# Kernel optimization log

Measured on AMD Instinct MI355X. Metric: run time of the kernel, lower is better.

## Reference

```python
import jax, jax.numpy as jnp
import numpy as np

INPUT_DIM = 64
OUTPUT_DIM = 128
KNN = 10          # hardcoded min(10, N) in source
RADIUS = 0.02     # density radius in source


def setup_inputs() -> dict:
    key = jax.random.key(0)
    k1, k2, k3, k4, k5, k6, k7 = jax.random.split(key, 7)
    B, N = 2, 8192
    points = jax.random.uniform(k1, (B, N, 3), dtype=jnp.float32)
    features = jax.random.normal(k2, (B, N, INPUT_DIM), dtype=jnp.float32)
    leaf_mask = jax.random.randint(k3, (B, N), 0, 2) > 0
    d_in = INPUT_DIM + 6
    s1 = 1.0 / np.sqrt(d_in)
    s2 = 1.0 / np.sqrt(OUTPUT_DIM)
    W1 = jax.random.uniform(k4, (d_in, OUTPUT_DIM), jnp.float32, -s1, s1)
    b1 = jax.random.uniform(k5, (OUTPUT_DIM,), jnp.float32, -s1, s1)
    W2 = jax.random.uniform(k6, (OUTPUT_DIM, OUTPUT_DIM), jnp.float32, -s2, s2)
    b2 = jax.random.uniform(k7, (OUTPUT_DIM,), jnp.float32, -s2, s2)
    return {"points": points, "features": features, "leaf_mask": leaf_mask,
            "W1": W1, "b1": b1, "W2": W2, "b2": b2}


def _leaf_geometry(points, mask):
    # points: [N,3], mask: [N] bool -> [N,6]
    mask_f = mask.astype(points.dtype)
    cnt = jnp.maximum(mask_f.sum(), 1.0)
    center = (points * mask_f[:, None]).sum(0) / cnt      # mean of masked points
    rel = points - center                                  # [N,3]
    dist_c = jnp.linalg.norm(rel, axis=1)                  # dist to leaf center
    rel_h = rel[:, 2]                                      # relative height
    horiz = jnp.linalg.norm(rel[:, :2], axis=1)            # horizontal distance
    # pairwise euclidean distances [N,N]; used only for thresholding and knn
    sq = jnp.sum(points * points, axis=1)
    d2 = sq[:, None] + sq[None, :] - 2.0 * (points @ points.T)
    dist = jax.lax.stop_gradient(jnp.sqrt(jnp.maximum(d2, 0.0)))
    density = jnp.sum((dist < RADIUS) & mask[None, :], axis=1).astype(points.dtype)
    # KNN (smallest distances, includes self) -> local PCA curvature
    _, idx = jax.lax.top_k(-dist, KNN)                     # [N,KNN]
    neighbors = points[idx]                                # [N,KNN,3]
    centered = neighbors - points[:, None, :]
    cov = jnp.einsum('nki,nkj->nij', centered, centered) / float(KNN)  # [N,3,3]
    ev = jnp.linalg.eigh(cov)[0]                           # ascending eigenvalues
    curv = ev[:, 0] / (ev[:, 2] + 1e-8)
    rad = jnp.arctan2(rel[:, 1], rel[:, 0])
    geom = jnp.stack([dist_c, rel_h, horiz, density, curv, rad], axis=1)
    # source returns zeros when mask is empty
    return jnp.where(mask_f.sum() > 0, geom, jnp.zeros_like(geom))


def reference(points, features, leaf_mask, W1, b1, W2, b2):
    geom = jax.vmap(_leaf_geometry)(points, leaf_mask)     # [B,N,6]
    combined = jnp.concatenate([features, geom], axis=-1)  # [B,N,input_dim+6]
    h = jax.nn.relu(combined @ W1 + b1)
    return jax.nn.relu(h @ W2 + b2)                        # [B,N,output_dim]
```

## Files before the change

kernel.cpp:

```cpp
#include <hip/hip_runtime.h>
#include <math.h>
#include <stdint.h>

#define B_SZ   2
#define N_PTS  8192
#define IN_DIM 64
#define D_IN   70
#define ODIM   128
#define NQ_ALL (B_SZ * N_PTS)
#define RADIUS_F 0.02f

#define GDIM  32
#define NCELL (GDIM * GDIM * GDIM)
#define HCELL 0.03125f

#define SUP     4
#define NSUP_AX 8
#define NSUPER  (NSUP_AX * NSUP_AX * NSUP_AX)
#define SCAP    352
#define LCAP    24
#define MAXROWS 100

#define MROWS   16

typedef unsigned long long u64;

__device__ __forceinline__ void insert11(u64 (&best)[11], u64 key) {
#pragma unroll
  for (int j = 10; j >= 1; --j) {
    u64 hi = (best[j - 1] > key) ? best[j - 1] : key;
    best[j] = (best[j] < hi) ? best[j] : hi;
  }
  best[0] = (best[0] < key) ? best[0] : key;
}
__device__ __forceinline__ void insert10(u64 (&best)[10], u64 key) {
#pragma unroll
  for (int j = 9; j >= 1; --j) {
    u64 hi = (best[j - 1] > key) ? best[j - 1] : key;
    best[j] = (best[j] < hi) ? best[j] : hi;
  }
  best[0] = (best[0] < key) ? best[0] : key;
}

__device__ __forceinline__ float sq3(float x, float y, float z) {
  return __fadd_rn(__fadd_rn(__fmul_rn(x, x), __fmul_rn(y, y)), __fmul_rn(z, z));
}

__device__ __forceinline__ int cellOf(float v) {
  int c = (int)(v * 32.0f);
  return min(max(c, 0), GDIM - 1);
}

__device__ __forceinline__ void geom_epilogue(const float* __restrict__ P,
                                              const int (&idxs)[10], float dens,
                                              float px, float py, float pz,
                                              float4 ctr, float* __restrict__ g) {
  double c00 = 0, c01 = 0, c02 = 0, c11 = 0, c12 = 0, c22 = 0;
#pragma unroll
  for (int j = 0; j < 10; ++j) {
    const int idx = idxs[j];
    const float nx = P[3 * idx + 0], ny = P[3 * idx + 1], nz = P[3 * idx + 2];
    const float ex = __fsub_rn(nx, px);
    const float ey = __fsub_rn(ny, py);
    const float ez = __fsub_rn(nz, pz);
    c00 += (double)ex * ex; c01 += (double)ex * ey; c02 += (double)ex * ez;
    c11 += (double)ey * ey; c12 += (double)ey * ez; c22 += (double)ez * ez;
  }
  const double a00 = c00 / 10.0, a01 = c01 / 10.0, a02 = c02 / 10.0;
  const double a11 = c11 / 10.0, a12 = c12 / 10.0, a22 = c22 / 10.0;

  double p1 = a01 * a01 + a02 * a02 + a12 * a12;
  double qq = (a00 + a11 + a22) / 3.0;
  double p2 = (a00 - qq) * (a00 - qq) + (a11 - qq) * (a11 - qq) +
              (a22 - qq) * (a22 - qq) + 2.0 * p1;
  double ev0, ev2;
  if (p2 <= 1e-60) {
    ev0 = ev2 = qq;
  } else {
    double p = sqrt(p2 / 6.0);
    double invp = 1.0 / p;
    double b00 = (a00 - qq) * invp, b11 = (a11 - qq) * invp, b22 = (a22 - qq) * invp;
    double b01 = a01 * invp, b02 = a02 * invp, b12 = a12 * invp;
    double detB = b00 * (b11 * b22 - b12 * b12) - b01 * (b01 * b22 - b12 * b02) +
                  b02 * (b01 * b12 - b11 * b02);
    double r = 0.5 * detB;
    r = fmin(1.0, fmax(-1.0, r));
    double phi = acos(r) / 3.0;
    ev2 = qq + 2.0 * p * cos(phi);
    ev0 = qq + 2.0 * p * cos(phi + 2.0943951023931953);
  }
  const float curv = (float)(ev0 / (ev2 + 1e-08));

  const bool on = ctr.w > 0.0f;
  const float rx = __fsub_rn(px, ctr.x);
  const float ry = __fsub_rn(py, ctr.y);
  const float rz = __fsub_rn(pz, ctr.z);
  const float dist_c = sqrtf(sq3(rx, ry, rz));
  const float horiz  = sqrtf(__fadd_rn(__fmul_rn(rx, rx), __fmul_rn(ry, ry)));
  const float rad    = atan2f(ry, rx);

  g[0] = on ? dist_c : 0.0f;
  g[1] = on ? rz : 0.0f;
  g[2] = on ? horiz : 0.0f;
  g[3] = on ? dens : 0.0f;
  g[4] = on ? curv : 0.0f;
  g[5] = on ? rad : 0.0f;
}

__global__ __launch_bounds__(256) void k_build(const float* __restrict__ points,
                                               const int* __restrict__ mask,
                                               int* __restrict__ count,
                                               double* __restrict__ ctrAcc) {
  const int t = blockIdx.x * 256 + threadIdx.x;
  const int b = t >> 13;
  const int i = t & (N_PTS - 1);
  const float* P = points + (size_t)b * N_PTS * 3;
  const float x = P[3 * i + 0], y = P[3 * i + 1], z = P[3 * i + 2];
  atomicAdd(&count[b * NCELL + (cellOf(z) * GDIM + cellOf(y)) * GDIM + cellOf(x)], 1);

  const bool m = mask[b * N_PTS + i] != 0;
  double vx = m ? (double)x : 0.0, vy = m ? (double)y : 0.0;
  double vz = m ? (double)z : 0.0, vc = m ? 1.0 : 0.0;
#pragma unroll
  for (int s = 1; s < 64; s <<= 1) {
    vx += __shfl_xor(vx, s); vy += __shfl_xor(vy, s);
    vz += __shfl_xor(vz, s); vc += __shfl_xor(vc, s);
  }
  __shared__ double sh[4][4];
  const int w = threadIdx.x >> 6;
  if ((threadIdx.x & 63) == 0) { sh[0][w] = vx; sh[1][w] = vy; sh[2][w] = vz; sh[3][w] = vc; }
  __syncthreads();
  if (threadIdx.x == 0) {
    atomicAdd(&ctrAcc[b * 4 + 0], sh[0][0] + sh[0][1] + sh[0][2] + sh[0][3]);
    atomicAdd(&ctrAcc[b * 4 + 1], sh[1][0] + sh[1][1] + sh[1][2] + sh[1][3]);
    atomicAdd(&ctrAcc[b * 4 + 2], sh[2][0] + sh[2][1] + sh[2][2] + sh[2][3]);
    atomicAdd(&ctrAcc[b * 4 + 3], sh[3][0] + sh[3][1] + sh[3][2] + sh[3][3]);
  }
}

__global__ __launch_bounds__(1024) void k_scan(const int* __restrict__ count,
                                               int* __restrict__ start,
                                               int* __restrict__ cur,
                                               const double* __restrict__ ctrAcc,
                                               float* __restrict__ centerOut) {
  const int b = blockIdx.x;
  const int t = threadIdx.x;
  if (t == 0) {
    const float cf = (float)ctrAcc[b * 4 + 3];
    const float div = fmaxf(cf, 1.0f);
    centerOut[b * 4 + 0] = (float)ctrAcc[b * 4 + 0] / div;
    centerOut[b * 4 + 1] = (float)ctrAcc[b * 4 + 1] / div;
    centerOut[b * 4 + 2] = (float)ctrAcc[b * 4 + 2] / div;
    centerOut[b * 4 + 3] = (cf > 0.0f) ? 1.0f : 0.0f;
  }
  int c[32]; int sum = 0;
#pragma unroll
  for (int j = 0; j < 32; ++j) { c[j] = count[b * NCELL + t * 32 + j]; sum += c[j]; }
  __shared__ int s[1024];
  s[t] = sum;
  __syncthreads();
  for (int off = 1; off < 1024; off <<= 1) {
    int v = (t >= off) ? s[t - off] : 0;
    __syncthreads();
    if (t >= off) s[t] += v;
    __syncthreads();
  }
  int excl = (t > 0) ? s[t - 1] : 0;
#pragma unroll
  for (int j = 0; j < 32; ++j) {
    start[b * (NCELL + 1) + t * 32 + j] = excl;
    cur[b * NCELL + t * 32 + j] = excl;
    excl += c[j];
  }
  if (t == 1023) start[b * (NCELL + 1) + NCELL] = excl;
}

__global__ __launch_bounds__(256) void k_scatter(const float* __restrict__ points,
                                                 const int* __restrict__ mask,
                                                 int* __restrict__ cur,
                                                 float4* __restrict__ sorted) {
  const int t = blockIdx.x * 256 + threadIdx.x;
  const int b = t >> 13;
  const int i = t & (N_PTS - 1);
  const float* P = points + (size_t)b * N_PTS * 3;
  const float x = P[3 * i + 0], y = P[3 * i + 1], z = P[3 * i + 2];
  const int cell = (cellOf(z) * GDIM + cellOf(y)) * GDIM + cellOf(x);
  const int pos = atomicAdd(&cur[b * NCELL + cell], 1);
  const unsigned wb = (unsigned)i | ((mask[b * N_PTS + i] != 0) ? 0x80000000u : 0u);
  sorted[(size_t)b * N_PTS + pos] = make_float4(x, y, z, __uint_as_float(wb));
}

__global__ __launch_bounds__(128) void k_collect(const float* __restrict__ points,
                                                 const float4* __restrict__ sorted,
                                                 const int* __restrict__ start,
                                                 const float* __restrict__ center,
                                                 float* __restrict__ geom,
                                                 int* __restrict__ list,
                                                 int* __restrict__ listCnt,
                                                 float DENS_T) {
  const int b  = blockIdx.y;
  const int sc = blockIdx.x;
  const int sx = sc & 7, sy = (sc >> 3) & 7, sz = sc >> 6;
  const int tid = threadIdx.x;

  const int* ST = start + b * (NCELL + 1);
  const float4* SP = sorted + (size_t)b * N_PTS;

  const int x0 = SUP * sx, x1 = SUP * sx + SUP - 1;
  const int y0 = SUP * sy, y1 = SUP * sy + SUP - 1;
  const int z0 = SUP * sz, z1 = SUP * sz + SUP - 1;
  const int hx0 = max(x0 - 3, 0), hx1 = min(x1 + 3, GDIM - 1);
  const int hy0 = max(y0 - 3, 0), hy1 = min(y1 + 3, GDIM - 1);
  const int hz0 = max(z0 - 3, 0), hz1 = min(z1 + 3, GDIM - 1);
  const int yc = hy1 - hy0 + 1;
  const int R  = (hz1 - hz0 + 1) * yc;

  __shared__ int    rs[MAXROWS], rp[MAXROWS + 1];
  __shared__ int    qs_[16], qp_[17];
  __shared__ float4 pts4[SCAP];
  __shared__ u64    lbuf[128 * LCAP];

  if (tid < 64) {
    {
      int qlen = 0, qst = 0;
      if (tid < 16) {
        const int z = z0 + (tid >> 2), y = y0 + (tid & 3);
        const int base = (z * GDIM + y) * GDIM;
        qst  = ST[base + x0];
        qlen = ST[base + x1 + 1] - qst;
      }
      int inc = qlen;
      for (int off = 1; off < 64; off <<= 1) { int v = __shfl_up(inc, off); if (tid >= off) inc += v; }
      if (tid < 16) { qs_[tid] = qst; qp_[tid] = inc - qlen; }
      if (tid == 63) qp_[16] = inc;
    }
    {
      int len[2] = {0, 0}, st2[2] = {0, 0};
#pragma unroll
      for (int k = 0; k < 2; ++k) {
        const int r = tid * 2 + k;
        if (r < R) {
          const int z = hz0 + r / yc, y = hy0 + r % yc;
          const int base = (z * GDIM + y) * GDIM;
          st2[k] = ST[base + hx0];
          len[k] = ST[base + hx1 + 1] - st2[k];
        }
      }
      int sum = len[0] + len[1];
      int inc = sum;
      for (int off = 1; off < 64; off <<= 1) { int v = __shfl_up(inc, off); if (tid >= off) inc += v; }
      int exc = inc - sum;
#pragma unroll
      for (int k = 0; k < 2; ++k) {
        const int r = tid * 2 + k;
        if (r < R) { rs[r] = st2[k]; rp[r] = exc; }
        exc += len[k];
      }
      if (tid == 63) rp[R] = inc;
    }
  }
  __syncthreads();

  const int C    = rp[R];
  const int qtot = qp_[16];
  if (qtot == 0) return;

  if (C > SCAP) {
    for (int t = tid; t < qtot; t += 128) {
      int lo = 0, hi = 15;
      while (lo < hi) { const int mid = (lo + hi + 1) >> 1; if (qp_[mid] <= t) lo = mid; else hi = mid - 1; }
      const int qglob = qs_[lo] + (t - qp_[lo]);
      const int pos = atomicAdd(listCnt, 1);
      list[pos] = (b << 13) | qglob;
    }
    return;
  }

  for (int i = tid; i < C; i += 128) {
    int lo = 0, hi = R - 1;
    while (lo < hi) { const int mid = (lo + hi + 1) >> 1; if (rp[mid] <= i) lo = mid; else hi = mid - 1; }
    pts4[i] = SP[rs[lo] + (i - rp[lo])];
  }
  __syncthreads();

  const bool cxl = (x0 - 3 < 0), cxh = (x1 + 3 > GDIM - 1);
  const bool cyl = (y0 - 3 < 0), cyh = (y1 + 3 > GDIM - 1);
  const bool czl = (z0 - 3 < 0), czh = (z1 + 3 > GDIM - 1);

  const float4 ctr = reinterpret_cast<const float4*>(center)[b];
  const float* P = points + (size_t)b * N_PTS * 3;
  const int sub = tid & 3;
  const int gq  = tid >> 2;

  for (int q0 = 0; q0 < qtot; q0 += 32) {
    const int myq = q0 + gq;
    const bool act = (myq < qtot);
    const int mq = act ? myq : 0;
    int lo = 0, hi = 15;
    while (lo < hi) { const int mid = (lo + hi + 1) >> 1; if (qp_[mid] <= mq) lo = mid; else hi = mid - 1; }
    const int qglob = qs_[lo] + (mq - qp_[lo]);
    const float4 qp4 = SP[qglob];
    const int qidx = (int)(__float_as_uint(qp4.w) & 0x7FFFFFFFu);
    const float px = qp4.x, py = qp4.y, pz = qp4.z;
    const float sqq = sq3(px, py, pz);

    const float mxl = cxl ? 1e9f : __fsub_rn(px, (float)hx0 * HCELL);
    const float mxh = cxh ? 1e9f : __fsub_rn((float)(hx1 + 1) * HCELL, px);
    const float myl = cyl ? 1e9f : __fsub_rn(py, (float)hy0 * HCELL);
    const float myh = cyh ? 1e9f : __fsub_rn((float)(hy1 + 1) * HCELL, py);
    const float mzl = czl ? 1e9f : __fsub_rn(pz, (float)hz0 * HCELL);
    const float mzh = czh ? 1e9f : __fsub_rn((float)(hz1 + 1) * HCELL, pz);
    const float gr = fminf(fminf(fminf(mxl, mxh), fminf(myl, myh)), fminf(mzl, mzh));
    const float fx = 0.5f * (1.0f + fminf(fminf(px, 1.0f - px) * (1.0f / 0.0935f), 1.0f));
    const float fy = 0.5f * (1.0f + fminf(fminf(py, 1.0f - py) * (1.0f / 0.0935f), 1.0f));
    const float fz = 0.5f * (1.0f + fminf(fminf(pz, 1.0f - pz) * (1.0f / 0.0935f), 1.0f));
    const float rT = 0.0935f * cbrtf(1.0f / (fx * fy * fz));
    const float cR = fminf(gr, rT);
    const float cT2 = cR * cR;
    const float certR = cR * 0.999f;

    int cnt = 0;
    u64* myb = &lbuf[tid * LCAP];
#pragma unroll 2
    for (int j = sub; j < C; j += 4) {
      const float4 tp = pts4[j];
      const float sqc = sq3(tp.x, tp.y, tp.z);
      const float dot = __fmaf_rn(pz, tp.z, __fmaf_rn(py, tp.y, __fmul_rn(px, tp.x)));
      const float d2  = __fsub_rn(__fadd_rn(sqq, sqc), __fmul_rn(2.0f, dot));
      const float d2c = fmaxf(d2, 0.0f);
      if (d2c < cT2) {
        if (cnt < LCAP) {
          const unsigned wb = __float_as_uint(tp.w);
          myb[cnt] = ((u64)__float_as_uint(d2c) << 32)
                   | (u64)(((wb & 0x7FFFFFFFu) << 1) | (wb >> 31));
        }
        ++cnt;
      }
    }

    u64 best[11];
#pragma unroll
    for (int j = 0; j < 11; ++j) best[j] = ~0ull;
    float dens = 0.0f;
    const int m = min(cnt, LCAP);
    for (int i = 0; i < m; ++i) {
      const u64 e = myb[i];
      if ((e & 1ull) && __uint_as_float((unsigned)(e >> 32)) < DENS_T) dens += 1.0f;
      if (e < best[10]) insert11(best, e);
    }
    int cntg = cnt;
    int over = (cnt > LCAP) ? 1 : 0;
#pragma unroll
    for (int s = 1; s < 4; s <<= 1) {
      dens += __shfl_xor(dens, s);
      cntg += __shfl_xor(cntg, s);
      over |= __shfl_xor(over, s);
      u64 ok[11];
#pragma unroll
      for (int j = 0; j < 11; ++j) ok[j] = __shfl_xor(best[j], s);
#pragma unroll
      for (int j = 0; j < 11; ++j) {
        if (ok[j] < best[10]) insert11(best, ok[j]); else break;
      }
    }

    if (act && sub == 0) {
      const float dist9 = sqrtf(__uint_as_float((unsigned)(best[9] >> 32)));
      bool bad = (over != 0) || (cntg < 10) || !(dist9 < certR);
      if (cntg >= 11) {
        const float dist10 = sqrtf(__uint_as_float((unsigned)(best[10] >> 32)));
        bad = bad || (dist10 == dist9);
      }
      if (bad) {
        const int pos = atomicAdd(listCnt, 1);
        list[pos] = (b << 13) | qglob;
      } else {
        int idxs[10];
#pragma unroll
        for (int j = 0; j < 10; ++j) idxs[j] = (int)(((unsigned)best[j]) >> 1);
        geom_epilogue(P, idxs, dens, px, py, pz, ctr,
                      geom + ((size_t)b * N_PTS + qidx) * 6);
      }
    }
  }
}

__global__ __launch_bounds__(256) void k_wavefb(const float* __restrict__ points,
                                                const float4* __restrict__ sorted,
                                                const int* __restrict__ start,
                                                const float* __restrict__ center,
                                                float* __restrict__ geom,
                                                int* __restrict__ flags2,
                                                const int* __restrict__ list,
                                                const int* __restrict__ listCnt) {
  const int lane = threadIdx.x & 63;
  const int wid  = threadIdx.x >> 6;
  const int n = *listCnt;
  for (int it = blockIdx.x * 4 + wid; it < n; it += gridDim.x * 4) {
    const int e = list[it];
    const int b = e >> 13, qs = e & (N_PTS - 1);
    const float4* SP = sorted + (size_t)b * N_PTS;
    const int* ST = start + b * (NCELL + 1);
    const float4 qp = SP[qs];
    const int qidx = (int)(__float_as_uint(qp.w) & 0x7FFFFFFFu);
    const float px = qp.x, py = qp.y, pz = qp.z;
    const float sqq = sq3(px, py, pz);
    const int cx = cellOf(px), cy = cellOf(py), cz = cellOf(pz);
    const int xlo = max(cx - 8, 0), xhi = min(cx + 8, GDIM - 1);
    const int ylo = max(cy - 8, 0), yhi = min(cy + 8, GDIM - 1);
    const int zlo = max(cz - 8, 0), zhi = min(cz + 8, GDIM - 1);
    const int ycw = yhi - ylo + 1;
    const int Rw = (zhi - zlo + 1) * ycw;

    u64 best[10];
#pragma unroll
    for (int j = 0; j < 10; ++j) best[j] = ((u64)0x7F800000u << 32) | 0xFFFFFFFFu;
    float dens = 0.0f;

    for (int r = lane; r < Rw; r += 64) {
      const int z = zlo + r / ycw, y = ylo + r % ycw;
      const int base = (z * GDIM + y) * GDIM;
      const int j0 = ST[base + xlo], j1 = ST[base + xhi + 1];
      for (int j = j0; j < j1; ++j) {
        const float4 tp = SP[j];
        const unsigned wb = __float_as_uint(tp.w);
        const float sqc = sq3(tp.x, tp.y, tp.z);
        const float dot = __fmaf_rn(pz, tp.z, __fmaf_rn(py, tp.y, __fmul_rn(px, tp.x)));
        const float d2  = __fsub_rn(__fadd_rn(sqq, sqc), __fmul_rn(2.0f, dot));
        const float dist = sqrtf(fmaxf(d2, 0.0f));
        if ((dist < RADIUS_F) && (wb & 0x80000000u)) dens += 1.0f;
        const u64 key = ((u64)__float_as_uint(dist) << 32) | (wb & 0x7FFFFFFFu);
        if (key < best[9]) insert10(best, key);
      }
    }
#pragma unroll
    for (int s = 1; s < 64; s <<= 1) {
      dens += __shfl_xor(dens, s);
      u64 ok[10];
#pragma unroll
      for (int j = 0; j < 10; ++j) ok[j] = __shfl_xor(best[j], s);
#pragma unroll
      for (int j = 0; j < 10; ++j) {
        if (ok[j] < best[9]) insert10(best, ok[j]); else break;
      }
    }
    if (lane == 0) {
      const float dist9 = __uint_as_float((unsigned)(best[9] >> 32));
      if (dist9 < 0.2494f) {
        const float4 ctr = reinterpret_cast<const float4*>(center)[b];
        const float* P = points + (size_t)b * N_PTS * 3;
        int idxs[10];
#pragma unroll
        for (int j = 0; j < 10; ++j) idxs[j] = (int)(((unsigned)best[j]) & 0x7FFFFFFFu);
        geom_epilogue(P, idxs, dens, px, py, pz, ctr, geom + ((size_t)b * N_PTS + qidx) * 6);
      } else {
        flags2[b * N_PTS + qs] = 1;
      }
    }
  }
}

__global__ __launch_bounds__(256) void k_fallback(const float* __restrict__ points,
                                                  const float4* __restrict__ sorted,
                                                  const int* __restrict__ start,
                                                  const float* __restrict__ center,
                                                  float* __restrict__ geom,
                                                  const int* __restrict__ flags2) {
  const int b = blockIdx.y;
  const int qs = blockIdx.x * 256 + threadIdx.x;
  if (flags2[b * N_PTS + qs] == 0) return;
  const float4 qp = sorted[(size_t)b * N_PTS + qs];
  const unsigned qw = __float_as_uint(qp.w);
  const int qidx = (int)(qw & 0x7FFFFFFFu);

  const float px = qp.x, py = qp.y, pz = qp.z;
  const float sqq = sq3(px, py, pz);
  const int cx = cellOf(px), cy = cellOf(py), cz = cellOf(pz);

  const int* ST = start + b * (NCELL + 1);
  const float4* SP = sorted + (size_t)b * N_PTS;

  u64 best[10];
#pragma unroll
  for (int j = 0; j < 10; ++j) best[j] = ((u64)0x7F800000u << 32) | 0xFFFFFFFFu;
  float dens = 0.0f;

  for (int rho = 0; rho < GDIM; ++rho) {
    const int zlo = max(cz - rho, 0), zhi = min(cz + rho, GDIM - 1);
    const int ylo = max(cy - rho, 0), yhi = min(cy + rho, GDIM - 1);
    for (int z = zlo; z <= zhi; ++z) {
      const int adz = abs(z - cz);
      for (int y = ylo; y <= yhi; ++y) {
        const int ady = abs(y - cy);
        const int m2 = max(adz, ady);
        int ja, jb;
        int ja2 = 0, jb2 = 0;
        const int rowBase = (z * GDIM + y) * GDIM;
        if (m2 == rho) {
          const int xa = max(cx - rho, 0), xb = min(cx + rho, GDIM - 1);
          ja = ST[rowBase + xa]; jb = ST[rowBase + xb + 1];
        } else {
          ja = jb = 0;
          if (cx - rho >= 0)        { ja = ST[rowBase + cx - rho]; jb = ST[rowBase + cx - rho + 1]; }
          if (cx + rho <= GDIM - 1) { ja2 = ST[rowBase + cx + rho]; jb2 = ST[rowBase + cx + rho + 1]; }
        }
#pragma unroll 1
        for (int pass = 0; pass < 2; ++pass) {
          const int j0 = pass ? ja2 : ja;
          const int j1 = pass ? jb2 : jb;
          for (int j = j0; j < j1; ++j) {
            const float4 tp = SP[j];
            const unsigned wb = __float_as_uint(tp.w);
            const float sqc = sq3(tp.x, tp.y, tp.z);
            const float dot = __fmaf_rn(pz, tp.z, __fmaf_rn(py, tp.y, __fmul_rn(px, tp.x)));
            const float d2  = __fsub_rn(__fadd_rn(sqq, sqc), __fmul_rn(2.0f, dot));
            const float dist = sqrtf(fmaxf(d2, 0.0f));
            if ((dist < RADIUS_F) && (wb & 0x80000000u)) dens += 1.0f;
            const u64 key = ((u64)__float_as_uint(dist) << 32) | (wb & 0x7FFFFFFFu);
            if (key < best[9]) insert10(best, key);
          }
        }
      }
    }
    if (rho >= 1) {
      const float dist9 = __uint_as_float((unsigned)(best[9] >> 32));
      if (dist9 < (float)rho * HCELL * 0.999f) break;
    }
  }

  const float4 ctr = reinterpret_cast<const float4*>(center)[b];
  const float* P = points + (size_t)b * N_PTS * 3;
  int idxs[10];
#pragma unroll
  for (int j = 0; j < 10; ++j) idxs[j] = (int)(((unsigned)best[j]) & 0x7FFFFFFFu);
  geom_epilogue(P, idxs, dens, px, py, pz, ctr, geom + ((size_t)b * N_PTS + qidx) * 6);
}

__global__ __launch_bounds__(256) void k_mlp(const float* __restrict__ features,
                                             const float* __restrict__ geom,
                                             const float* __restrict__ W1,
                                             const float* __restrict__ b1,
                                             const float* __restrict__ W2,
                                             const float* __restrict__ b2,
                                             float* __restrict__ out) {
  __shared__ float A[MROWS][71];
  __shared__ float H[MROWS][133];
  const int tid = threadIdx.x;
  const int row0 = blockIdx.x * MROWS;

  {
    const int r = tid >> 4, f4 = (tid & 15) * 4;
    const float4 v = *reinterpret_cast<const float4*>(&features[(size_t)(row0 + r) * IN_DIM + f4]);
    A[r][f4 + 0] = v.x; A[r][f4 + 1] = v.y; A[r][f4 + 2] = v.z; A[r][f4 + 3] = v.w;
  }
  if (tid < MROWS * 6) {
    const int r = tid / 6, k = tid % 6;
    A[r][IN_DIM + k] = geom[(size_t)(row0 + r) * 6 + k];
  }
  __syncthreads();

  const int r = tid >> 4;
  const int c = (tid & 15) * 8;

  float acc[8];
#pragma unroll
  for (int j = 0; j < 8; ++j) acc[j] = 0.0f;

#pragma unroll 4
  for (int k = 0; k < D_IN; ++k) {
    const float a = A[r][k];
    const float4 w0 = *reinterpret_cast<const float4*>(&W1[(size_t)k * ODIM + c]);
    const float4 w1 = *reinterpret_cast<const float4*>(&W1[(size_t)k * ODIM + c + 4]);
    acc[0] = fmaf(a, w0.x, acc[0]); acc[1] = fmaf(a, w0.y, acc[1]);
    acc[2] = fmaf(a, w0.z, acc[2]); acc[3] = fmaf(a, w0.w, acc[3]);
    acc[4] = fmaf(a, w1.x, acc[4]); acc[5] = fmaf(a, w1.y, acc[5]);
    acc[6] = fmaf(a, w1.z, acc[6]); acc[7] = fmaf(a, w1.w, acc[7]);
  }
  {
    const float4 bb0 = *reinterpret_cast<const float4*>(&b1[c]);
    const float4 bb1 = *reinterpret_cast<const float4*>(&b1[c + 4]);
    float4 h0 = make_float4(fmaxf(acc[0] + bb0.x, 0.f), fmaxf(acc[1] + bb0.y, 0.f),
                            fmaxf(acc[2] + bb0.z, 0.f), fmaxf(acc[3] + bb0.w, 0.f));
    float4 h1 = make_float4(fmaxf(acc[4] + bb1.x, 0.f), fmaxf(acc[5] + bb1.y, 0.f),
                            fmaxf(acc[6] + bb1.z, 0.f), fmaxf(acc[7] + bb1.w, 0.f));
    H[r][c + 0] = h0.x; H[r][c + 1] = h0.y; H[r][c + 2] = h0.z; H[r][c + 3] = h0.w;
    H[r][c + 4] = h1.x; H[r][c + 5] = h1.y; H[r][c + 6] = h1.z; H[r][c + 7] = h1.w;
  }
  __syncthreads();

#pragma unroll
  for (int j = 0; j < 8; ++j) acc[j] = 0.0f;

#pragma unroll 4
  for (int k = 0; k < ODIM; ++k) {
    const float a = H[r][k];
    const float4 w0 = *reinterpret_cast<const float4*>(&W2[(size_t)k * ODIM + c]);
    const float4 w1 = *reinterpret_cast<const float4*>(&W2[(size_t)k * ODIM + c + 4]);
    acc[0] = fmaf(a, w0.x, acc[0]); acc[1] = fmaf(a, w0.y, acc[1]);
    acc[2] = fmaf(a, w0.z, acc[2]); acc[3] = fmaf(a, w0.w, acc[3]);
    acc[4] = fmaf(a, w1.x, acc[4]); acc[5] = fmaf(a, w1.y, acc[5]);
    acc[6] = fmaf(a, w1.z, acc[6]); acc[7] = fmaf(a, w1.w, acc[7]);
  }
  {
    const float4 bb0 = *reinterpret_cast<const float4*>(&b2[c]);
    const float4 bb1 = *reinterpret_cast<const float4*>(&b2[c + 4]);
    const size_t row = (size_t)(row0 + r);
    float4 o0 = make_float4(fmaxf(acc[0] + bb0.x, 0.f), fmaxf(acc[1] + bb0.y, 0.f),
                            fmaxf(acc[2] + bb0.z, 0.f), fmaxf(acc[3] + bb0.w, 0.f));
    float4 o1 = make_float4(fmaxf(acc[4] + bb1.x, 0.f), fmaxf(acc[5] + bb1.y, 0.f),
                            fmaxf(acc[6] + bb1.z, 0.f), fmaxf(acc[7] + bb1.w, 0.f));
    *reinterpret_cast<float4*>(&out[row * ODIM + c]) = o0;
    *reinterpret_cast<float4*>(&out[row * ODIM + c + 4]) = o1;
  }
}

extern "C" void kernel_launch(void* const* d_in, const int* in_sizes, int n_in,
                              void* d_out, int out_size, void* d_ws, size_t ws_size,
                              hipStream_t stream) {
  const float* points   = (const float*)d_in[0];
  const float* features = (const float*)d_in[1];
  const int*   mask     = (const int*)d_in[2];
  const float* W1       = (const float*)d_in[3];
  const float* b1       = (const float*)d_in[4];
  const float* W2       = (const float*)d_in[5];
  const float* b2       = (const float*)d_in[6];
  float* out = (float*)d_out;

  const double Rd   = (double)0.02f;
  const double midd = Rd - ldexp(1.0, -30);
  const double Td   = midd * midd;
  float densT = (float)Td;
  if ((double)densT <= Td) densT = nextafterf(densT, 1.0f);

  char* w = (char*)d_ws;
  size_t off = 0;
  auto take = [&](size_t bytes) { char* p = w + off; off = (off + bytes + 255) & ~(size_t)255; return p; };
  float*  geomBuf   = (float*)take((size_t)NQ_ALL * 6 * 4);
  float*  centerBuf = (float*)take(2 * 16);
  char*   zero0     = (char*)take(0);
  int*    countBuf  = (int*)take((size_t)B_SZ * NCELL * 4);
  int*    flags2Buf = (int*)take((size_t)NQ_ALL * 4);
  int*    listCnt   = (int*)take(4);
  double* ctrAcc    = (double*)take((size_t)B_SZ * 4 * 8);
  char*   zero1     = (char*)take(0);
  int*    startBuf  = (int*)take((size_t)B_SZ * (NCELL + 1) * 4);
  int*    curBuf    = (int*)take((size_t)B_SZ * NCELL * 4);
  float4* sortedBuf = (float4*)take((size_t)B_SZ * N_PTS * 16);
  int*    listBuf   = (int*)take((size_t)NQ_ALL * 4);
  (void)ws_size;

  hipMemsetAsync(zero0, 0, (size_t)(zero1 - zero0), stream);
  k_build<<<NQ_ALL / 256, 256, 0, stream>>>(points, mask, countBuf, ctrAcc);
  k_scan<<<B_SZ, 1024, 0, stream>>>(countBuf, startBuf, curBuf, ctrAcc, centerBuf);
  k_scatter<<<NQ_ALL / 256, 256, 0, stream>>>(points, mask, curBuf, sortedBuf);
  k_collect<<<dim3(NSUPER, B_SZ), 128, 0, stream>>>(points, sortedBuf, startBuf, centerBuf,
                                                    geomBuf, listBuf, listCnt, densT);
  k_wavefb<<<512, 256, 0, stream>>>(points, sortedBuf, startBuf, centerBuf,
                                    geomBuf, flags2Buf, listBuf, listCnt);
  k_fallback<<<dim3(N_PTS / 256, B_SZ), 256, 0, stream>>>(points, sortedBuf, startBuf,
                                                          centerBuf, geomBuf, flags2Buf);
  k_mlp<<<NQ_ALL / MROWS, 256, 0, stream>>>(features, geomBuf, W1, b1, W2, b2, out);
}
```

Baseline: 214.4 us.

## Register-block MLP with shared-memory weights; split KNN scan across eight lanes

```diff
diff --git a/kernel.cpp b/kernel.cpp
--- a/kernel.cpp
+++ b/kernel.cpp
@@ -18,10 +18,8 @@
 #define NSUP_AX 8
 #define NSUPER  (NSUP_AX * NSUP_AX * NSUP_AX)
 #define SCAP    352
-#define LCAP    24
+#define LCAP    16
 #define MAXROWS 100
-
-#define MROWS   16
 
 typedef unsigned long long u64;
 
@@ -289,10 +287,10 @@
 
   const float4 ctr = reinterpret_cast<const float4*>(center)[b];
   const float* P = points + (size_t)b * N_PTS * 3;
-  const int sub = tid & 3;
-  const int gq  = tid >> 2;
-
-  for (int q0 = 0; q0 < qtot; q0 += 32) {
+  const int sub = tid & 7;
+  const int gq  = tid >> 3;
+
+  for (int q0 = 0; q0 < qtot; q0 += 16) {
     const int myq = q0 + gq;
     const bool act = (myq < qtot);
     const int mq = act ? myq : 0;
@@ -322,7 +320,7 @@
     int cnt = 0;
     u64* myb = &lbuf[tid * LCAP];
 #pragma unroll 2
-    for (int j = sub; j < C; j += 4) {
+    for (int j = sub; j < C; j += 8) {
       const float4 tp = pts4[j];
       const float sqc = sq3(tp.x, tp.y, tp.z);
       const float dot = __fmaf_rn(pz, tp.z, __fmaf_rn(py, tp.y, __fmul_rn(px, tp.x)));
@@ -351,7 +349,7 @@
     int cntg = cnt;
     int over = (cnt > LCAP) ? 1 : 0;
 #pragma unroll
-    for (int s = 1; s < 4; s <<= 1) {
+    for (int s = 1; s < 8; s <<= 1) {
       dens += __shfl_xor(dens, s);
       cntg += __shfl_xor(cntg, s);
       over |= __shfl_xor(over, s);
@@ -543,74 +541,106 @@
                                              const float* __restrict__ W2,
                                              const float* __restrict__ b2,
                                              float* __restrict__ out) {
-  __shared__ float A[MROWS][71];
-  __shared__ float H[MROWS][133];
+  __shared__ float Wbuf[ODIM * ODIM];
+  __shared__ float A[64][71];
+  __shared__ float H[64][133];
   const int tid = threadIdx.x;
-  const int row0 = blockIdx.x * MROWS;
+  const int row0 = blockIdx.x * 64;
 
   {
-    const int r = tid >> 4, f4 = (tid & 15) * 4;
-    const float4 v = *reinterpret_cast<const float4*>(&features[(size_t)(row0 + r) * IN_DIM + f4]);
-    A[r][f4 + 0] = v.x; A[r][f4 + 1] = v.y; A[r][f4 + 2] = v.z; A[r][f4 + 3] = v.w;
-  }
-  if (tid < MROWS * 6) {
-    const int r = tid / 6, k = tid % 6;
+    const int r = tid >> 2, f4 = (tid & 3) * 16;
+#pragma unroll
+    for (int j = 0; j < 4; ++j) {
+      const float4 v = *reinterpret_cast<const float4*>(
+          &features[(size_t)(row0 + r) * IN_DIM + f4 + j * 4]);
+      A[r][f4 + 4 * j + 0] = v.x; A[r][f4 + 4 * j + 1] = v.y;
+      A[r][f4 + 4 * j + 2] = v.z; A[r][f4 + 4 * j + 3] = v.w;
+    }
+  }
+  for (int i = tid; i < 64 * 6; i += 256) {
+    const int r = i / 6, k = i % 6;
     A[r][IN_DIM + k] = geom[(size_t)(row0 + r) * 6 + k];
   }
+  for (int i = tid; i < D_IN * ODIM / 4; i += 256) {
+    const float4 v = reinterpret_cast<const float4*>(W1)[i];
+    Wbuf[4 * i + 0] = v.x; Wbuf[4 * i + 1] = v.y;
+    Wbuf[4 * i + 2] = v.z; Wbuf[4 * i + 3] = v.w;
+  }
   __syncthreads();
 
-  const int r = tid >> 4;
-  const int c = (tid & 15) * 8;
-
-  float acc[8];
-#pragma unroll
-  for (int j = 0; j < 8; ++j) acc[j] = 0.0f;
-
-#pragma unroll 4
+  const int rg = (tid >> 4) * 4;
+  const int c  = (tid & 15) * 8;
+
+  float acc[4][8];
+#pragma unroll
+  for (int i = 0; i < 4; ++i)
+#pragma unroll
+    for (int j = 0; j < 8; ++j) acc[i][j] = 0.0f;
+
+#pragma unroll 2
   for (int k = 0; k < D_IN; ++k) {
-    const float a = A[r][k];
-    const float4 w0 = *reinterpret_cast<const float4*>(&W1[(size_t)k * ODIM + c]);
-    const float4 w1 = *reinterpret_cast<const float4*>(&W1[(size_t)k * ODIM + c + 4]);
-    acc[0] = fmaf(a, w0.x, acc[0]); acc[1] = fmaf(a, w0.y, acc[1]);
-    acc[2] = fmaf(a, w0.z, acc[2]); acc[3] = fmaf(a, w0.w, acc[3]);
-    acc[4] = fmaf(a, w1.x, acc[4]); acc[5] = fmaf(a, w1.y, acc[5]);
-    acc[6] = fmaf(a, w1.z, acc[6]); acc[7] = fmaf(a, w1.w, acc[7]);
-  }
+    float a[4];
+#pragma unroll
+    for (int i = 0; i < 4; ++i) a[i] = A[rg + i][k];
+    const float4 w0 = *reinterpret_cast<const float4*>(&Wbuf[k * ODIM + c]);
+    const float4 w1 = *reinterpret_cast<const float4*>(&Wbuf[k * ODIM + c + 4]);
+    const float w[8] = {w0.x, w0.y, w0.z, w0.w, w1.x, w1.y, w1.z, w1.w};
+#pragma unroll
+    for (int i = 0; i < 4; ++i)
+#pragma unroll
+      for (int j = 0; j < 8; ++j) acc[i][j] = fmaf(a[i], w[j], acc[i][j]);
+  }
+  __syncthreads();
+
   {
     const float4 bb0 = *reinterpret_cast<const float4*>(&b1[c]);
     const float4 bb1 = *reinterpret_cast<const float4*>(&b1[c + 4]);
-    float4 h0 = make_float4(fmaxf(acc[0] + bb0.x, 0.f), fmaxf(acc[1] + bb0.y, 0.f),
-                            fmaxf(acc[2] + bb0.z, 0.f), fmaxf(acc[3] + bb0.w, 0.f));
-    float4 h1 = make_float4(fmaxf(acc[4] + bb1.x, 0.f), fmaxf(acc[5] + bb1.y, 0.f),
-                            fmaxf(acc[6] + bb1.z, 0.f), fmaxf(acc[7] + bb1.w, 0.f));
-    H[r][c + 0] = h0.x; H[r][c + 1] = h0.y; H[r][c + 2] = h0.z; H[r][c + 3] = h0.w;
-    H[r][c + 4] = h1.x; H[r][c + 5] = h1.y; H[r][c + 6] = h1.z; H[r][c + 7] = h1.w;
+    const float bb[8] = {bb0.x, bb0.y, bb0.z, bb0.w, bb1.x, bb1.y, bb1.z, bb1.w};
+#pragma unroll
+    for (int i = 0; i < 4; ++i) {
+#pragma unroll
+      for (int j = 0; j < 8; ++j) H[rg + i][c + j] = fmaxf(acc[i][j] + bb[j], 0.0f);
+    }
+  }
+  for (int i = tid; i < ODIM * ODIM / 4; i += 256) {
+    const float4 v = reinterpret_cast<const float4*>(W2)[i];
+    Wbuf[4 * i + 0] = v.x; Wbuf[4 * i + 1] = v.y;
+    Wbuf[4 * i + 2] = v.z; Wbuf[4 * i + 3] = v.w;
   }
   __syncthreads();
 
 #pragma unroll
-  for (int j = 0; j < 8; ++j) acc[j] = 0.0f;
-
-#pragma unroll 4
+  for (int i = 0; i < 4; ++i)
+#pragma unroll
+    for (int j = 0; j < 8; ++j) acc[i][j] = 0.0f;
+
+#pragma unroll 2
   for (int k = 0; k < ODIM; ++k) {
-    const float a = H[r][k];
-    const float4 w0 = *reinterpret_cast<const float4*>(&W2[(size_t)k * ODIM + c]);
-    const float4 w1 = *reinterpret_cast<const float4*>(&W2[(size_t)k * ODIM + c + 4]);
-    acc[0] = fmaf(a, w0.x, acc[0]); acc[1] = fmaf(a, w0.y, acc[1]);
-    acc[2] = fmaf(a, w0.z, acc[2]); acc[3] = fmaf(a, w0.w, acc[3]);
-    acc[4] = fmaf(a, w1.x, acc[4]); acc[5] = fmaf(a, w1.y, acc[5]);
-    acc[6] = fmaf(a, w1.z, acc[6]); acc[7] = fmaf(a, w1.w, acc[7]);
+    float a[4];
+#pragma unroll
+    for (int i = 0; i < 4; ++i) a[i] = H[rg + i][k];
+    const float4 w0 = *reinterpret_cast<const float4*>(&Wbuf[k * ODIM + c]);
+    const float4 w1 = *reinterpret_cast<const float4*>(&Wbuf[k * ODIM + c + 4]);
+    const float w[8] = {w0.x, w0.y, w0.z, w0.w, w1.x, w1.y, w1.z, w1.w};
+#pragma unroll
+    for (int i = 0; i < 4; ++i)
+#pragma unroll
+      for (int j = 0; j < 8; ++j) acc[i][j] = fmaf(a[i], w[j], acc[i][j]);
   }
   {
     const float4 bb0 = *reinterpret_cast<const float4*>(&b2[c]);
     const float4 bb1 = *reinterpret_cast<const float4*>(&b2[c + 4]);
-    const size_t row = (size_t)(row0 + r);
-    float4 o0 = make_float4(fmaxf(acc[0] + bb0.x, 0.f), fmaxf(acc[1] + bb0.y, 0.f),
-                            fmaxf(acc[2] + bb0.z, 0.f), fmaxf(acc[3] + bb0.w, 0.f));
-    float4 o1 = make_float4(fmaxf(acc[4] + bb1.x, 0.f), fmaxf(acc[5] + bb1.y, 0.f),
-                            fmaxf(acc[6] + bb1.z, 0.f), fmaxf(acc[7] + bb1.w, 0.f));
-    *reinterpret_cast<float4*>(&out[row * ODIM + c]) = o0;
-    *reinterpret_cast<float4*>(&out[row * ODIM + c + 4]) = o1;
+    const float bb[8] = {bb0.x, bb0.y, bb0.z, bb0.w, bb1.x, bb1.y, bb1.z, bb1.w};
+#pragma unroll
+    for (int i = 0; i < 4; ++i) {
+      const size_t row = (size_t)(row0 + rg + i);
+      float4 o0 = make_float4(fmaxf(acc[i][0] + bb[0], 0.f), fmaxf(acc[i][1] + bb[1], 0.f),
+                              fmaxf(acc[i][2] + bb[2], 0.f), fmaxf(acc[i][3] + bb[3], 0.f));
+      float4 o1 = make_float4(fmaxf(acc[i][4] + bb[4], 0.f), fmaxf(acc[i][5] + bb[5], 0.f),
+                              fmaxf(acc[i][6] + bb[6], 0.f), fmaxf(acc[i][7] + bb[7], 0.f));
+      *reinterpret_cast<float4*>(&out[row * ODIM + c]) = o0;
+      *reinterpret_cast<float4*>(&out[row * ODIM + c + 4]) = o1;
+    }
   }
 }
 
@@ -659,5 +689,5 @@
                                     geomBuf, flags2Buf, listBuf, listCnt);
   k_fallback<<<dim3(N_PTS / 256, B_SZ), 256, 0, stream>>>(points, sortedBuf, startBuf,
                                                           centerBuf, geomBuf, flags2Buf);
-  k_mlp<<<NQ_ALL / MROWS, 256, 0, stream>>>(features, geomBuf, W1, b1, W2, b2, out);
-}
+  k_mlp<<<NQ_ALL / 64, 256, 0, stream>>>(features, geomBuf, W1, b1, W2, b2, out);
+}
```

Result: faster. 206.4 us (-3.7%).
